# Kernel optimization log

Hardware: AMD Instinct MI355X
Metric: run time of the kernel (lower is better)

Reference implementation:

```python
import jax, jax.numpy as jnp
import numpy as np

N_VERTS = 20000
BATCH = 4
C_FEAT = 64
VOX = 64
N_FACES = 40000


def _lin(key, fan_in, fan_out):
    return jax.random.normal(key, (fan_in, fan_out), jnp.float32) / np.sqrt(fan_in)


def setup_inputs() -> dict:
    key = jax.random.key(0)
    ks = jax.random.split(key, 16)
    # faces -> unique directed edges, as in faces_to_edges (done host-side, static shape)
    rng = np.random.default_rng(0)
    faces = rng.integers(0, N_VERTS, (N_FACES, 3))
    e = np.concatenate([faces[:, :2], faces[:, 1:], faces[:, [0, 2]]], axis=0)
    e = np.unique(e, axis=0)
    edge_index = jnp.asarray(e.T, dtype=jnp.int32)  # [2, E]
    gdims = [(128, 256), (256, 512), (512, 1024), (1024, 512), (512, 256), (256, 128)]
    inp = {
        'features': jax.random.normal(ks[0], (BATCH, C_FEAT, VOX, VOX, VOX), jnp.float32),
        'vertices': jax.random.normal(ks[1], (N_VERTS, 3), jnp.float32),
        'edge_index': edge_index,
        'enc_W1': _lin(ks[2], 3 + C_FEAT, 256), 'enc_b1': jnp.zeros((256,), jnp.float32),
        'enc_W2': _lin(ks[3], 256, 128), 'enc_b2': jnp.zeros((128,), jnp.float32),
    }
    for i, (a, b) in enumerate(gdims):
        inp[f'gW{i+1}'] = _lin(ks[4 + i], a, b)
        inp[f'gb{i+1}'] = jnp.zeros((b,), jnp.float32)
    inp['hW1'] = _lin(ks[10], 128, 128); inp['hb1'] = jnp.zeros((128,), jnp.float32)
    inp['hW2'] = _lin(ks[11], 128, 64); inp['hb2'] = jnp.zeros((64,), jnp.float32)
    inp['hW3'] = _lin(ks[12], 64, 3); inp['hb3'] = jnp.zeros((3,), jnp.float32)
    return inp


def trilinear_sample(feat, grid):
    # feat [B,C,D,H,W]; grid [B,N,3] in [-1,1], channel order (x->W, y->H, z->D)
    # align_corners=True, padding_mode='border'
    _, C, D, H, W = feat.shape

    def per_sample(f, g):
        def un(c, s):
            return jnp.clip((c + 1.0) * 0.5 * (s - 1), 0.0, s - 1.0)
        x = un(g[:, 0], W); y = un(g[:, 1], H); z = un(g[:, 2], D)
        x0 = jnp.floor(x); y0 = jnp.floor(y); z0 = jnp.floor(z)
        wx = x - x0; wy = y - y0; wz = z - z0
        x0i = jnp.clip(x0.astype(jnp.int32), 0, W - 1); x1i = jnp.clip(x0i + 1, 0, W - 1)
        y0i = jnp.clip(y0.astype(jnp.int32), 0, H - 1); y1i = jnp.clip(y0i + 1, 0, H - 1)
        z0i = jnp.clip(z0.astype(jnp.int32), 0, D - 1); z1i = jnp.clip(z0i + 1, 0, D - 1)
        def g8(zi, yi, xi):
            return f[:, zi, yi, xi]  # [C,N]
        c00 = g8(z0i, y0i, x0i) * (1 - wx) + g8(z0i, y0i, x1i) * wx
        c01 = g8(z0i, y1i, x0i) * (1 - wx) + g8(z0i, y1i, x1i) * wx
        c10 = g8(z1i, y0i, x0i) * (1 - wx) + g8(z1i, y0i, x1i) * wx
        c11 = g8(z1i, y1i, x0i) * (1 - wx) + g8(z1i, y1i, x1i) * wx
        c0 = c00 * (1 - wy) + c01 * wy
        c1 = c10 * (1 - wy) + c11 * wy
        return (c0 * (1 - wz) + c1 * wz).T  # [N,C]

    return jax.vmap(per_sample)(feat, grid)


def _forward(features, vertices, edge_index,
             enc_W1, enc_b1, enc_W2, enc_b2,
             gWs, gbs, hW1, hb1, hW2, hb2, hW3, hb3):
    B = features.shape[0]
    N = vertices.shape[0]
    # sample_voxel_features: min/max over batch axis of identical copies -> constant grid
    vexp = jnp.broadcast_to(vertices[None], (B, N, 3))
    mn = vexp.min(axis=0, keepdims=True)
    mx = vexp.max(axis=0, keepdims=True)
    vn = 2.0 * (vexp - mn) / (mx - mn + 1e-6) - 1.0
    vn = vn / 1.5  # chamber == 0
    vfeat = trilinear_sample(features, vn)  # [B,N,C]
    x = jnp.concatenate([vexp, vfeat], axis=-1)
    x = jax.nn.relu(x @ enc_W1 + enc_b1)
    x = jax.nn.relu(x @ enc_W2 + enc_b2)  # [B,N,128]
    # PyG GCNConv: self-loops + symmetric normalization (bn layers unused in source forward)
    src = edge_index[0]
    dst = edge_index[1]
    deg = jnp.zeros((N,), x.dtype).at[dst].add(1.0) + 1.0  # includes self-loop
    dinv = 1.0 / jnp.sqrt(deg)
    nrm = dinv[src] * dinv[dst]  # [E]
    selfw = (dinv * dinv)[None, :, None]  # self-loop norm

    def gcn(h, W_, b_):
        h = h @ W_  # [B,N,Cout]
        agg = jnp.zeros_like(h).at[:, dst].add(h[:, src] * nrm[None, :, None])
        return jax.nn.relu(h * selfw + agg + b_)

    for W_, b_ in zip(gWs, gbs):
        x = gcn(x, W_, b_)
    d = jax.nn.relu(x @ hW1 + hb1)
    d = jax.nn.relu(d @ hW2 + hb2)
    d = jnp.tanh(d @ hW3 + hb3)
    d = jnp.nan_to_num(d, nan=0.0)
    return vertices[None] + jnp.clip(d, -2.5, 2.5)


def reference(features, vertices, edge_index,
              enc_W1, enc_b1, enc_W2, enc_b2,
              gW1, gb1, gW2, gb2, gW3, gb3, gW4, gb4, gW5, gb5, gW6, gb6,
              hW1, hb1, hW2, hb2, hW3, hb3):
    return _forward(features, vertices, edge_index,
                    enc_W1, enc_b1, enc_W2, enc_b2,
                    (gW1, gW2, gW3, gW4, gW5, gW6),
                    (gb1, gb2, gb3, gb4, gb5, gb6),
                    hW1, hb1, hW2, hb2, hW3, hb3)
```

## Files before the change

### kernel.cpp

```cpp
#include <hip/hip_runtime.h>
#include <math.h>

#define NV 20000
#define NV_PAD 20096
#define NB 4
#define M_TOTAL (NB * NV_PAD)
#define CF 64
#define VX 64

typedef short short8 __attribute__((ext_vector_type(8)));
typedef float floatx4 __attribute__((ext_vector_type(4)));

__device__ __forceinline__ float bf2f(unsigned int h) {
  return __uint_as_float(h << 16);
}
__device__ __forceinline__ unsigned short f2bf(float f) {
  unsigned int u = __float_as_uint(f);
  u += 0x7fffu + ((u >> 16) & 1u);
  return (unsigned short)(u >> 16);
}


__global__ void hist_dst_kernel(const int* __restrict__ dst, int E, int* __restrict__ cnt) {
  int i = blockIdx.x * blockDim.x + threadIdx.x;
  if (i < E) atomicAdd(&cnt[dst[i]], 1);
}

__global__ void scan_kernel(const int* __restrict__ cnt, int* __restrict__ rowp,
                            float* __restrict__ dinv, int n) {
  __shared__ int sdata[1024];
  __shared__ int run_s;
  if (threadIdx.x == 0) run_s = 0;
  __syncthreads();
  for (int base = 0; base < n; base += 1024) {
    int i = base + (int)threadIdx.x;
    int v = (i < n) ? cnt[i] : 0;
    sdata[threadIdx.x] = v;
    __syncthreads();
    int run = run_s;
    for (int ofs = 1; ofs < 1024; ofs <<= 1) {
      int t = (threadIdx.x >= (unsigned)ofs) ? sdata[threadIdx.x - ofs] : 0;
      __syncthreads();
      sdata[threadIdx.x] += t;
      __syncthreads();
    }
    if (i < n) {
      rowp[i] = run + sdata[threadIdx.x] - v;
      dinv[i] = 1.0f / sqrtf((float)(v + 1));
    }
    if (threadIdx.x == 1023) run_s = run + sdata[1023];
    __syncthreads();
  }
  if (threadIdx.x == 0) rowp[n] = run_s;
}

__global__ void fill_csr_kernel(const int* __restrict__ src, const int* __restrict__ dst, int E,
                                const int* __restrict__ rowp, int* __restrict__ cnt2,
                                const float* __restrict__ dinv,
                                int* __restrict__ esrc, float* __restrict__ dsrc) {
  int i = blockIdx.x * blockDim.x + threadIdx.x;
  if (i < E) {
    int d = dst[i];
    int s = src[i];
    int pos = rowp[d] + atomicAdd(&cnt2[d], 1);
    esrc[pos] = s;
    dsrc[pos] = dinv[s];
  }
}

__global__ void dinvrep_kernel(const float* __restrict__ dinv, float* __restrict__ drep) {
  int idx = blockIdx.x * blockDim.x + threadIdx.x;
  if (idx >= M_TOTAL) return;
  int n = idx % NV_PAD;
  drep[idx] = (n < NV) ? dinv[n] : 1.0f;
}

__global__ void vfeat_kernel(const float* __restrict__ feat, float* __restrict__ vfeat) {
  int t = blockIdx.x * blockDim.x + threadIdx.x;
  if (t >= NB * CF) return;
  float c = (2.0f * 0.0f / 1e-6f - 1.0f) / 1.5f;
  float pos = (c + 1.0f) * 0.5f * (float)(VX - 1);
  pos = fminf(fmaxf(pos, 0.0f), (float)(VX - 1));
  float f0 = floorf(pos);
  float w = pos - f0;
  int i0 = (int)f0;
  int i1 = i0 + 1; if (i1 > VX - 1) i1 = VX - 1;
  const float* base = feat + (size_t)t * VX * VX * VX;
  float wz[2] = {1.0f - w, w};
  int   iz[2] = {i0, i1};
  float acc = 0.0f;
  #pragma unroll
  for (int a = 0; a < 2; ++a)
    #pragma unroll
    for (int b = 0; b < 2; ++b)
      #pragma unroll
      for (int d = 0; d < 2; ++d)
        acc += wz[a] * wz[b] * wz[d] * base[(size_t)iz[a] * VX * VX + iz[b] * VX + iz[d]];
  vfeat[t] = acc;
}

__global__ void encconst_kernel(const float* __restrict__ vfeat, const float* __restrict__ W1,
                                const float* __restrict__ b1, float* __restrict__ encc) {
  int idx = blockIdx.x * blockDim.x + threadIdx.x;
  if (idx >= NB * 256) return;
  int b = idx >> 8, j = idx & 255;
  float acc = b1[j];
  #pragma unroll 8
  for (int c = 0; c < CF; ++c) acc += vfeat[b * CF + c] * W1[(3 + c) * 256 + j];
  encc[idx] = acc;
}

__global__ void enc1_kernel(const float* __restrict__ verts, const float* __restrict__ W1,
                            const float* __restrict__ encc, unsigned short* __restrict__ out) {
  int idx = blockIdx.x * blockDim.x + threadIdx.x;
  if (idx >= NV * 256) return;
  int n = idx >> 8, j = idx & 255;
  int b = blockIdx.y;
  float acc = encc[b * 256 + j]
            + verts[n * 3 + 0] * W1[0 * 256 + j]
            + verts[n * 3 + 1] * W1[1 * 256 + j]
            + verts[n * 3 + 2] * W1[2 * 256 + j];
  out[((size_t)(b * NV_PAD + n)) * 256 + j] = f2bf(fmaxf(acc, 0.0f));
}

struct WPrep {
  const float* src[9];
  unsigned short* dst[9];
};

__global__ void wprep_all_kernel(WPrep wp) {
  const int WKc[9] = {256, 128, 256, 512, 1024, 512, 256, 128, 128};
  const int WNc[9] = {128, 256, 512, 1024, 512, 256, 128, 128, 64};
  const int cum[10] = {0, 32768, 65536, 196608, 720896, 1245184, 1376256, 1409024, 1425408, 1433600};
  int idx = blockIdx.x * blockDim.x + threadIdx.x;
  if (idx >= 1433600) return;
  #pragma unroll
  for (int s = 0; s < 9; ++s) {
    if (idx >= cum[s] && idx < cum[s + 1]) {
      int local = idx - cum[s];
      int k = local / WNc[s];
      int n = local - k * WNc[s];
      wp.dst[s][(size_t)n * WKc[s] + k] = f2bf(wp.src[s][local]);
      return;
    }
  }
}

#define BM 128
#define BN 128
#define BK 32

__launch_bounds__(256, 4)
__global__ void gemm_bt_kernel(const unsigned short* __restrict__ A,
                               const unsigned short* __restrict__ Bt,
                               const float* __restrict__ bias,
                               const float* __restrict__ rowscale,
                               unsigned short* __restrict__ C,
                               int K, int Nreal, int flags) {
  __shared__ unsigned short As[BM * BK];
  __shared__ unsigned short Bs[BN * BK];
  int tid = threadIdx.x;
  int wave = tid >> 6, lane = tid & 63;

  unsigned int nwg = gridDim.x * gridDim.y;
  unsigned int orig = blockIdx.y * gridDim.x + blockIdx.x;
  unsigned int xcd = orig & 7u, pos = orig >> 3;
  unsigned int q = nwg >> 3, r = nwg & 7u;
  unsigned int wgid = (xcd < r ? xcd * (q + 1u) : r * (q + 1u) + (xcd - r) * q) + pos;
  unsigned int bx = wgid % gridDim.x;
  unsigned int by = wgid / gridDim.x;

  int mbase = by * BM;
  int nbase = bx * BN;
  int wm = (wave >> 1) * 64, wn = (wave & 1) * 64;

  floatx4 acc[4][4] = {};

  const int rowS = wave * 16 + (lane >> 2);
  const int sswz = ((lane >> 2) + (lane >> 4)) & 3;
  const int kseg = (((lane & 3) ^ sswz) << 3);
  const int fr = lane & 15, fq = lane >> 4;
  const int fswz = (fr + (fr >> 2)) & 3;
  const int fchunk = ((fq ^ fswz) << 3);

  for (int kb = 0; kb < K; kb += BK) {
    #pragma unroll
    for (int p = 0; p < 2; ++p) {
      const unsigned short* ga = A + (size_t)(mbase + rowS + p * 64) * K + kb + kseg;
      __builtin_amdgcn_global_load_lds(
          (const __attribute__((address_space(1))) void*)ga,
          (__attribute__((address_space(3))) void*)(As + wave * 512 + p * 2048), 16, 0, 0);
      const unsigned short* gb = Bt + (size_t)(nbase + rowS + p * 64) * K + kb + kseg;
      __builtin_amdgcn_global_load_lds(
          (const __attribute__((address_space(1))) void*)gb,
          (__attribute__((address_space(3))) void*)(Bs + wave * 512 + p * 2048), 16, 0, 0);
    }
    __syncthreads();
    short8 af[4], bf[4];
    #pragma unroll
    for (int i = 0; i < 4; ++i)
      af[i] = *(const short8*)(As + (wm + i * 16 + fr) * BK + fchunk);
    #pragma unroll
    for (int j = 0; j < 4; ++j)
      bf[j] = *(const short8*)(Bs + (wn + j * 16 + fr) * BK + fchunk);
    #pragma unroll
    for (int i = 0; i < 4; ++i)
      #pragma unroll
      for (int j = 0; j < 4; ++j)
        acc[i][j] = __builtin_amdgcn_mfma_f32_16x16x32_bf16(af[i], bf[j], acc[i][j], 0, 0, 0);
    __syncthreads();
  }

  #pragma unroll
  for (int j = 0; j < 4; ++j) {
    int n = nbase + wn + j * 16 + fr;
    if (n >= Nreal) continue;
    float bv = (flags & 1) ? bias[n] : 0.0f;
    #pragma unroll
    for (int i = 0; i < 4; ++i) {
      #pragma unroll
      for (int r = 0; r < 4; ++r) {
        int m = mbase + wm + i * 16 + fq * 4 + r;
        float v = acc[i][j][r];
        if (flags & 4) v *= rowscale[m];
        v += bv;
        if (flags & 2) v = fmaxf(v, 0.0f);
        C[(size_t)m * Nreal + n] = f2bf(v);
      }
    }
  }
}

__global__ void gcn_gather_kernel(const uint4* __restrict__ hs8,
                                  const float* __restrict__ bias,
                                  const float* __restrict__ dinv,
                                  const int* __restrict__ rowp, const int* __restrict__ esrc,
                                  uint4* __restrict__ out, int lc8) {
  int idx = blockIdx.x * blockDim.x + threadIdx.x;
  int C8 = 1 << lc8;
  if (idx >= NV * C8) return;
  int n = idx >> lc8;
  int j = idx & (C8 - 1);
  size_t rowbase = (size_t)blockIdx.y * NV_PAD;
  uint4 u = hs8[((rowbase + n) << lc8) + j];
  float a0 = bf2f(u.x & 0xffff), a1 = bf2f(u.x >> 16);
  float a2 = bf2f(u.y & 0xffff), a3 = bf2f(u.y >> 16);
  float a4 = bf2f(u.z & 0xffff), a5 = bf2f(u.z >> 16);
  float a6 = bf2f(u.w & 0xffff), a7 = bf2f(u.w >> 16);
  int s = rowp[n], e = rowp[n + 1];
  int t = s;
  int src = (t < e) ? esrc[t] : 0;
  while (t < e) {
    uint4 v = hs8[((rowbase + src) << lc8) + j];
    ++t;
    int src_n = (t < e) ? esrc[t] : 0;
    a0 += bf2f(v.x & 0xffff); a1 += bf2f(v.x >> 16);
    a2 += bf2f(v.y & 0xffff); a3 += bf2f(v.y >> 16);
    a4 += bf2f(v.z & 0xffff); a5 += bf2f(v.z >> 16);
    a6 += bf2f(v.w & 0xffff); a7 += bf2f(v.w >> 16);
    src = src_n;
  }
  float dn = dinv[n];
  int j8 = j << 3;
  a0 = fmaxf(a0 * dn + bias[j8 + 0], 0.0f);
  a1 = fmaxf(a1 * dn + bias[j8 + 1], 0.0f);
  a2 = fmaxf(a2 * dn + bias[j8 + 2], 0.0f);
  a3 = fmaxf(a3 * dn + bias[j8 + 3], 0.0f);
  a4 = fmaxf(a4 * dn + bias[j8 + 4], 0.0f);
  a5 = fmaxf(a5 * dn + bias[j8 + 5], 0.0f);
  a6 = fmaxf(a6 * dn + bias[j8 + 6], 0.0f);
  a7 = fmaxf(a7 * dn + bias[j8 + 7], 0.0f);
  uint4 o;
  o.x = (unsigned int)f2bf(a0) | ((unsigned int)f2bf(a1) << 16);
  o.y = (unsigned int)f2bf(a2) | ((unsigned int)f2bf(a3) << 16);
  o.z = (unsigned int)f2bf(a4) | ((unsigned int)f2bf(a5) << 16);
  o.w = (unsigned int)f2bf(a6) | ((unsigned int)f2bf(a7) << 16);
  out[((rowbase + n) << lc8) + j] = o;
}

__global__ void gcn_pre_gather_kernel(const uint4* __restrict__ x8,
                                      const float* __restrict__ dinv,
                                      const int* __restrict__ rowp, const int* __restrict__ esrc,
                                      const float* __restrict__ dsrc,
                                      uint4* __restrict__ out, int lc8) {
  int idx = blockIdx.x * blockDim.x + threadIdx.x;
  int C8 = 1 << lc8;
  if (idx >= NV * C8) return;
  int n = idx >> lc8;
  int j = idx & (C8 - 1);
  size_t rowbase = (size_t)blockIdx.y * NV_PAD;
  float dn = dinv[n];
  uint4 u = x8[((rowbase + n) << lc8) + j];
  float a0 = dn * bf2f(u.x & 0xffff), a1 = dn * bf2f(u.x >> 16);
  float a2 = dn * bf2f(u.y & 0xffff), a3 = dn * bf2f(u.y >> 16);
  float a4 = dn * bf2f(u.z & 0xffff), a5 = dn * bf2f(u.z >> 16);
  float a6 = dn * bf2f(u.w & 0xffff), a7 = dn * bf2f(u.w >> 16);
  int s = rowp[n], e = rowp[n + 1];
  int t = s;
  int src = (t < e) ? esrc[t] : 0;
  float w = (t < e) ? dsrc[t] : 0.0f;
  while (t < e) {
    uint4 v = x8[((rowbase + src) << lc8) + j];
    float wv = w;
    ++t;
    src = (t < e) ? esrc[t] : 0;
    w = (t < e) ? dsrc[t] : 0.0f;
    a0 += wv * bf2f(v.x & 0xffff); a1 += wv * bf2f(v.x >> 16);
    a2 += wv * bf2f(v.y & 0xffff); a3 += wv * bf2f(v.y >> 16);
    a4 += wv * bf2f(v.z & 0xffff); a5 += wv * bf2f(v.z >> 16);
    a6 += wv * bf2f(v.w & 0xffff); a7 += wv * bf2f(v.w >> 16);
  }
  a0 *= dn; a1 *= dn; a2 *= dn; a3 *= dn;
  a4 *= dn; a5 *= dn; a6 *= dn; a7 *= dn;
  uint4 o;
  o.x = (unsigned int)f2bf(a0) | ((unsigned int)f2bf(a1) << 16);
  o.y = (unsigned int)f2bf(a2) | ((unsigned int)f2bf(a3) << 16);
  o.z = (unsigned int)f2bf(a4) | ((unsigned int)f2bf(a5) << 16);
  o.w = (unsigned int)f2bf(a6) | ((unsigned int)f2bf(a7) << 16);
  out[((rowbase + n) << lc8) + j] = o;
}

__global__ void head3_kernel(const unsigned short* __restrict__ d, const float* __restrict__ hW3,
                             const float* __restrict__ hb3, const float* __restrict__ verts,
                             float* __restrict__ out) {
  int idx = blockIdx.x * blockDim.x + threadIdx.x;
  if (idx >= NV * 3) return;
  int n = idx / 3;
  int k = idx - n * 3;
  int b = blockIdx.y;
  const unsigned short* drow = d + ((size_t)(b * NV_PAD + n)) * 64;
  float acc = hb3[k];
  #pragma unroll 8
  for (int c = 0; c < 64; ++c) acc += bf2f(drow[c]) * hW3[c * 3 + k];
  float t = tanhf(acc);
  t = fminf(fmaxf(t, -2.5f), 2.5f);
  out[(size_t)b * NV * 3 + idx] = verts[idx] + t;
}


static inline void launch_gemm(const unsigned short* A, const unsigned short* Bt,
                               const float* bias, const float* rowscale, unsigned short* C,
                               int N, int K, int flags, hipStream_t stream) {
  int Npad = (N + BN - 1) / BN * BN;
  dim3 grid(Npad / BN, M_TOTAL / BM);
  gemm_bt_kernel<<<grid, 256, 0, stream>>>(A, Bt, bias, rowscale, C, K, N, flags);
}

extern "C" void kernel_launch(void* const* d_in, const int* in_sizes, int n_in,
                              void* d_out, int out_size, void* d_ws, size_t ws_size,
                              hipStream_t stream) {
  const float* features = (const float*)d_in[0];
  const float* vertices = (const float*)d_in[1];
  const int* edge_index = (const int*)d_in[2];
  const int E = in_sizes[2] / 2;
  const int* esrc_in = edge_index;
  const int* edst_in = edge_index + E;
  const float* enc_W1 = (const float*)d_in[3];
  const float* enc_b1 = (const float*)d_in[4];
  const float* enc_W2 = (const float*)d_in[5];
  const float* enc_b2 = (const float*)d_in[6];
  const float* gW[6]; const float* gb[6];
  for (int i = 0; i < 6; ++i) { gW[i] = (const float*)d_in[7 + 2 * i]; gb[i] = (const float*)d_in[8 + 2 * i]; }
  const float* hW1 = (const float*)d_in[19]; const float* hb1 = (const float*)d_in[20];
  const float* hW2 = (const float*)d_in[21]; const float* hb2 = (const float*)d_in[22];
  const float* hW3 = (const float*)d_in[23]; const float* hb3 = (const float*)d_in[24];

  char* ws = (char*)d_ws;
  size_t off = 0;
  auto alloc = [&](size_t bytes) -> void* {
    void* p = (void*)(ws + off);
    off += (bytes + 255) & ~(size_t)255;
    return p;
  };
  unsigned short* bufA = (unsigned short*)alloc((size_t)M_TOTAL * 1024 * 2);
  unsigned short* bufB = (unsigned short*)alloc((size_t)M_TOTAL * 1024 * 2);
  float* dinv  = (float*)alloc(NV * sizeof(float));
  float* drep  = (float*)alloc(M_TOTAL * sizeof(float));
  float* vfeat = (float*)alloc(NB * CF * sizeof(float));
  float* encc  = (float*)alloc(NB * 256 * sizeof(float));
  int* cnt  = (int*)alloc(NV * sizeof(int));
  int* rowp = (int*)alloc((NV + 1) * sizeof(int));
  int* cnt2 = (int*)alloc(NV * sizeof(int));
  int* esrc = (int*)alloc((size_t)E * sizeof(int));
  float* dsrc = (float*)alloc((size_t)E * sizeof(float));
  const size_t wtsz[9] = {128 * 256, 256 * 128, 512 * 256, 1024 * 512, 512 * 1024,
                          256 * 512, 128 * 256, 128 * 128, 128 * 128};
  unsigned short* wt[9];
  {
    size_t tot = 0;
    for (int i = 0; i < 9; ++i) tot += wtsz[i];
    unsigned short* base = (unsigned short*)alloc(tot * 2);
    size_t o = 0;
    for (int i = 0; i < 9; ++i) { wt[i] = base + o; o += wtsz[i]; }
  }

  hipMemsetAsync(cnt,  0, NV * sizeof(int), stream);
  hipMemsetAsync(cnt2, 0, NV * sizeof(int), stream);
  hist_dst_kernel<<<(E + 255) / 256, 256, 0, stream>>>(edst_in, E, cnt);
  scan_kernel<<<1, 1024, 0, stream>>>(cnt, rowp, dinv, NV);
  fill_csr_kernel<<<(E + 255) / 256, 256, 0, stream>>>(esrc_in, edst_in, E, rowp, cnt2,
                                                       dinv, esrc, dsrc);
  dinvrep_kernel<<<(M_TOTAL + 255) / 256, 256, 0, stream>>>(dinv, drep);
  vfeat_kernel<<<1, 256, 0, stream>>>(features, vfeat);
  encconst_kernel<<<NB, 256, 0, stream>>>(vfeat, enc_W1, enc_b1, encc);

  WPrep wp;
  const float* wsrc[9] = {enc_W2, gW[0], gW[1], gW[2], gW[3], gW[4], gW[5], hW1, hW2};
  for (int i = 0; i < 9; ++i) { wp.src[i] = wsrc[i]; wp.dst[i] = wt[i]; }
  wprep_all_kernel<<<(1433600 + 255) / 256, 256, 0, stream>>>(wp);

  const int gout[6] = {256, 512, 1024, 512, 256, 128};
  const int gin[6]  = {128, 256, 512, 1024, 512, 256};
  const int inlc8[6] = {4, 5, 6, 7, 6, 5};
  const int outlc8[6] = {5, 6, 7, 6, 5, 4};
  const int inside[6] = {1, 1, 1, 0, 0, 0};

  dim3 e1grid((NV * 256 + 255) / 256, NB);
  enc1_kernel<<<e1grid, 256, 0, stream>>>(vertices, enc_W1, encc, bufA);
  launch_gemm(bufA, wt[0], enc_b2, nullptr, bufB, 128, 256, 1 | 2, stream);

  unsigned short* x = bufB;
  unsigned short* h = bufA;
  for (int i = 0; i < 6; ++i) {
    if (inside[i]) {
      int total8 = NV * (gin[i] / 8);
      dim3 pgrid((total8 + 255) / 256, NB);
      gcn_pre_gather_kernel<<<pgrid, 256, 0, stream>>>(
          (const uint4*)x, dinv, rowp, esrc, dsrc, (uint4*)h, inlc8[i]);
      launch_gemm(h, wt[1 + i], gb[i], nullptr, x, gout[i], gin[i], 1 | 2, stream);
    } else {
      launch_gemm(x, wt[1 + i], nullptr, drep, h, gout[i], gin[i], 4, stream);
      int total8 = NV * (gout[i] / 8);
      dim3 ggrid((total8 + 255) / 256, NB);
      gcn_gather_kernel<<<ggrid, 256, 0, stream>>>(
          (const uint4*)h, gb[i], dinv, rowp, esrc, (uint4*)x, outlc8[i]);
    }
  }
  launch_gemm(x, wt[7], hb1, nullptr, h, 128, 128, 1 | 2, stream);
  launch_gemm(h, wt[8], hb2, nullptr, x, 64, 128, 1 | 2, stream);
  dim3 hgrid((NV * 3 + 255) / 256, NB);
  head3_kernel<<<hgrid, 256, 0, stream>>>(x, hW3, hb3, vertices, (float*)d_out);
}
```

Measured before the change: 1.177 ms.

## Double-buffer GEMM LDS tiles and batch-fuse GCN gather kernels

The GEMM kernel now double-buffers its A/B LDS tiles, issuing the global-to-LDS loads for the next K step before computing on the current one. This hides load latency and leaves one barrier per iteration instead of two, at the cost of doubled LDS use, which may lower occupancy. Both GCN gather kernels now have each thread handle all four batch items, so CSR row pointers, edge indices and weights are read once per vertex instead of once per batch. The batch grid dimension is removed in exchange for more registers per thread and fewer threads in flight.

```diff
diff --git a/kernel.cpp b/kernel.cpp
--- a/kernel.cpp
+++ b/kernel.cpp
@@ -157,8 +157,8 @@
                                const float* __restrict__ rowscale,
                                unsigned short* __restrict__ C,
                                int K, int Nreal, int flags) {
-  __shared__ unsigned short As[BM * BK];
-  __shared__ unsigned short Bs[BN * BK];
+  __shared__ unsigned short As[2 * BM * BK];
+  __shared__ unsigned short Bs[2 * BM * BK];
   int tid = threadIdx.x;
   int wave = tid >> 6, lane = tid & 63;
 
@@ -183,32 +183,45 @@
   const int fswz = (fr + (fr >> 2)) & 3;
   const int fchunk = ((fq ^ fswz) << 3);
 
-  for (int kb = 0; kb < K; kb += BK) {
+  const unsigned short* ga0 = A + (size_t)(mbase + rowS) * K + kseg;
+  const unsigned short* gb0 = Bt + (size_t)(nbase + rowS) * K + kseg;
+
+  auto stage = [&](int kb, int half) {
     #pragma unroll
     for (int p = 0; p < 2; ++p) {
-      const unsigned short* ga = A + (size_t)(mbase + rowS + p * 64) * K + kb + kseg;
       __builtin_amdgcn_global_load_lds(
-          (const __attribute__((address_space(1))) void*)ga,
-          (__attribute__((address_space(3))) void*)(As + wave * 512 + p * 2048), 16, 0, 0);
-      const unsigned short* gb = Bt + (size_t)(nbase + rowS + p * 64) * K + kb + kseg;
+          (const __attribute__((address_space(1))) void*)(ga0 + (size_t)(p * 64) * K + kb),
+          (__attribute__((address_space(3))) void*)(As + half * 4096 + wave * 512 + p * 2048),
+          16, 0, 0);
       __builtin_amdgcn_global_load_lds(
-          (const __attribute__((address_space(1))) void*)gb,
-          (__attribute__((address_space(3))) void*)(Bs + wave * 512 + p * 2048), 16, 0, 0);
+          (const __attribute__((address_space(1))) void*)(gb0 + (size_t)(p * 64) * K + kb),
+          (__attribute__((address_space(3))) void*)(Bs + half * 4096 + wave * 512 + p * 2048),
+          16, 0, 0);
     }
-    __syncthreads();
+  };
+
+  const int nt = K / BK;
+  stage(0, 0);
+  __syncthreads();
+  int cur = 0;
+  for (int t = 0; t < nt; ++t) {
+    if (t + 1 < nt) stage((t + 1) * BK, cur ^ 1);
+    const unsigned short* as = As + cur * 4096;
+    const unsigned short* bs = Bs + cur * 4096;
     short8 af[4], bf[4];
     #pragma unroll
     for (int i = 0; i < 4; ++i)
-      af[i] = *(const short8*)(As + (wm + i * 16 + fr) * BK + fchunk);
+      af[i] = *(const short8*)(as + (wm + i * 16 + fr) * BK + fchunk);
     #pragma unroll
     for (int j = 0; j < 4; ++j)
-      bf[j] = *(const short8*)(Bs + (wn + j * 16 + fr) * BK + fchunk);
+      bf[j] = *(const short8*)(bs + (wn + j * 16 + fr) * BK + fchunk);
     #pragma unroll
     for (int i = 0; i < 4; ++i)
       #pragma unroll
       for (int j = 0; j < 4; ++j)
         acc[i][j] = __builtin_amdgcn_mfma_f32_16x16x32_bf16(af[i], bf[j], acc[i][j], 0, 0, 0);
     __syncthreads();
+    cur ^= 1;
   }
 
   #pragma unroll
@@ -241,41 +254,66 @@
   if (idx >= NV * C8) return;
   int n = idx >> lc8;
   int j = idx & (C8 - 1);
-  size_t rowbase = (size_t)blockIdx.y * NV_PAD;
-  uint4 u = hs8[((rowbase + n) << lc8) + j];
-  float a0 = bf2f(u.x & 0xffff), a1 = bf2f(u.x >> 16);
-  float a2 = bf2f(u.y & 0xffff), a3 = bf2f(u.y >> 16);
-  float a4 = bf2f(u.z & 0xffff), a5 = bf2f(u.z >> 16);
-  float a6 = bf2f(u.w & 0xffff), a7 = bf2f(u.w >> 16);
+  const size_t bstride = (size_t)NV_PAD << lc8;
+  float a[NB][8];
+  #pragma unroll
+  for (int b = 0; b < NB; ++b) {
+    uint4 u = hs8[b * bstride + ((size_t)n << lc8) + j];
+    a[b][0] = bf2f(u.x & 0xffff); a[b][1] = bf2f(u.x >> 16);
+    a[b][2] = bf2f(u.y & 0xffff); a[b][3] = bf2f(u.y >> 16);
+    a[b][4] = bf2f(u.z & 0xffff); a[b][5] = bf2f(u.z >> 16);
+    a[b][6] = bf2f(u.w & 0xffff); a[b][7] = bf2f(u.w >> 16);
+  }
   int s = rowp[n], e = rowp[n + 1];
   int t = s;
   int src = (t < e) ? esrc[t] : 0;
   while (t < e) {
-    uint4 v = hs8[((rowbase + src) << lc8) + j];
+    size_t rb = ((size_t)src << lc8) + j;
+    uint4 v0 = hs8[rb];
+    uint4 v1 = hs8[rb + bstride];
+    uint4 v2 = hs8[rb + 2 * bstride];
+    uint4 v3 = hs8[rb + 3 * bstride];
     ++t;
-    int src_n = (t < e) ? esrc[t] : 0;
-    a0 += bf2f(v.x & 0xffff); a1 += bf2f(v.x >> 16);
-    a2 += bf2f(v.y & 0xffff); a3 += bf2f(v.y >> 16);
-    a4 += bf2f(v.z & 0xffff); a5 += bf2f(v.z >> 16);
-    a6 += bf2f(v.w & 0xffff); a7 += bf2f(v.w >> 16);
-    src = src_n;
+    src = (t < e) ? esrc[t] : 0;
+    a[0][0] += bf2f(v0.x & 0xffff); a[0][1] += bf2f(v0.x >> 16);
+    a[0][2] += bf2f(v0.y & 0xffff); a[0][3] += bf2f(v0.y >> 16);
+    a[0][4] += bf2f(v0.z & 0xffff); a[0][5] += bf2f(v0.z >> 16);
+    a[0][6] += bf2f(v0.w & 0xffff); a[0][7] += bf2f(v0.w >> 16);
+    a[1][0] += bf2f(v1.x & 0xffff); a[1][1] += bf2f(v1.x >> 16);
+    a[1][2] += bf2f(v1.y & 0xffff); a[1][3] += bf2f(v1.y >> 16);
+    a[1][4] += bf2f(v1.z & 0xffff); a[1][5] += bf2f(v1.z >> 16);
+    a[1][6] += bf2f(v1.w & 0xffff); a[1][7] += bf2f(v1.w >> 16);
+    a[2][0] += bf2f(v2.x & 0xffff); a[2][1] += bf2f(v2.x >> 16);
+    a[2][2] += bf2f(v2.y & 0xffff); a[2][3] += bf2f(v2.y >> 16);
+    a[2][4] += bf2f(v2.z & 0xffff); a[2][5] += bf2f(v2.z >> 16);
+    a[2][6] += bf2f(v2.w & 0xffff); a[2][7] += bf2f(v2.w >> 16);
+    a[3][0] += bf2f(v3.x & 0xffff); a[3][1] += bf2f(v3.x >> 16);
+    a[3][2] += bf2f(v3.y & 0xffff); a[3][3] += bf2f(v3.y >> 16);
+    a[3][4] += bf2f(v3.z & 0xffff); a[3][5] += bf2f(v3.z >> 16);
+    a[3][6] += bf2f(v3.w & 0xffff); a[3][7] += bf2f(v3.w >> 16);
   }
   float dn = dinv[n];
   int j8 = j << 3;
-  a0 = fmaxf(a0 * dn + bias[j8 + 0], 0.0f);
-  a1 = fmaxf(a1 * dn + bias[j8 + 1], 0.0f);
-  a2 = fmaxf(a2 * dn + bias[j8 + 2], 0.0f);
-  a3 = fmaxf(a3 * dn + bias[j8 + 3], 0.0f);
-  a4 = fmaxf(a4 * dn + bias[j8 + 4], 0.0f);
-  a5 = fmaxf(a5 * dn + bias[j8 + 5], 0.0f);
-  a6 = fmaxf(a6 * dn + bias[j8 + 6], 0.0f);
-  a7 = fmaxf(a7 * dn + bias[j8 + 7], 0.0f);
-  uint4 o;
-  o.x = (unsigned int)f2bf(a0) | ((unsigned int)f2bf(a1) << 16);
-  o.y = (unsigned int)f2bf(a2) | ((unsigned int)f2bf(a3) << 16);
-  o.z = (unsigned int)f2bf(a4) | ((unsigned int)f2bf(a5) << 16);
-  o.w = (unsigned int)f2bf(a6) | ((unsigned int)f2bf(a7) << 16);
-  out[((rowbase + n) << lc8) + j] = o;
+  float bb[8];
+  #pragma unroll
+  for (int c = 0; c < 8; ++c) bb[c] = bias[j8 + c];
+  #pragma unroll
+  for (int b = 0; b < NB; ++b) {
+    uint4 o;
+    float r0 = fmaxf(a[b][0] * dn + bb[0], 0.0f);
+    float r1 = fmaxf(a[b][1] * dn + bb[1], 0.0f);
+    float r2 = fmaxf(a[b][2] * dn + bb[2], 0.0f);
+    float r3 = fmaxf(a[b][3] * dn + bb[3], 0.0f);
+    float r4 = fmaxf(a[b][4] * dn + bb[4], 0.0f);
+    float r5 = fmaxf(a[b][5] * dn + bb[5], 0.0f);
+    float r6 = fmaxf(a[b][6] * dn + bb[6], 0.0f);
+    float r7 = fmaxf(a[b][7] * dn + bb[7], 0.0f);
+    o.x = (unsigned int)f2bf(r0) | ((unsigned int)f2bf(r1) << 16);
+    o.y = (unsigned int)f2bf(r2) | ((unsigned int)f2bf(r3) << 16);
+    o.z = (unsigned int)f2bf(r4) | ((unsigned int)f2bf(r5) << 16);
+    o.w = (unsigned int)f2bf(r6) | ((unsigned int)f2bf(r7) << 16);
+    out[b * bstride + ((size_t)n << lc8) + j] = o;
+  }
 }
 
 __global__ void gcn_pre_gather_kernel(const uint4* __restrict__ x8,
@@ -288,36 +326,57 @@
   if (idx >= NV * C8) return;
   int n = idx >> lc8;
   int j = idx & (C8 - 1);
-  size_t rowbase = (size_t)blockIdx.y * NV_PAD;
+  const size_t bstride = (size_t)NV_PAD << lc8;
   float dn = dinv[n];
-  uint4 u = x8[((rowbase + n) << lc8) + j];
-  float a0 = dn * bf2f(u.x & 0xffff), a1 = dn * bf2f(u.x >> 16);
-  float a2 = dn * bf2f(u.y & 0xffff), a3 = dn * bf2f(u.y >> 16);
-  float a4 = dn * bf2f(u.z & 0xffff), a5 = dn * bf2f(u.z >> 16);
-  float a6 = dn * bf2f(u.w & 0xffff), a7 = dn * bf2f(u.w >> 16);
+  float a[NB][8];
+  #pragma unroll
+  for (int b = 0; b < NB; ++b) {
+    uint4 u = x8[b * bstride + ((size_t)n << lc8) + j];
+    a[b][0] = dn * bf2f(u.x & 0xffff); a[b][1] = dn * bf2f(u.x >> 16);
+    a[b][2] = dn * bf2f(u.y & 0xffff); a[b][3] = dn * bf2f(u.y >> 16);
+    a[b][4] = dn * bf2f(u.z & 0xffff); a[b][5] = dn * bf2f(u.z >> 16);
+    a[b][6] = dn * bf2f(u.w & 0xffff); a[b][7] = dn * bf2f(u.w >> 16);
+  }
   int s = rowp[n], e = rowp[n + 1];
   int t = s;
   int src = (t < e) ? esrc[t] : 0;
   float w = (t < e) ? dsrc[t] : 0.0f;
   while (t < e) {
-    uint4 v = x8[((rowbase + src) << lc8) + j];
+    size_t rb = ((size_t)src << lc8) + j;
+    uint4 v0 = x8[rb];
+    uint4 v1 = x8[rb + bstride];
+    uint4 v2 = x8[rb + 2 * bstride];
+    uint4 v3 = x8[rb + 3 * bstride];
     float wv = w;
     ++t;
     src = (t < e) ? esrc[t] : 0;
     w = (t < e) ? dsrc[t] : 0.0f;
-    a0 += wv * bf2f(v.x & 0xffff); a1 += wv * bf2f(v.x >> 16);
-    a2 += wv * bf2f(v.y & 0xffff); a3 += wv * bf2f(v.y >> 16);
-    a4 += wv * bf2f(v.z & 0xffff); a5 += wv * bf2f(v.z >> 16);
-    a6 += wv * bf2f(v.w & 0xffff); a7 += wv * bf2f(v.w >> 16);
-  }
-  a0 *= dn; a1 *= dn; a2 *= dn; a3 *= dn;
-  a4 *= dn; a5 *= dn; a6 *= dn; a7 *= dn;
-  uint4 o;
-  o.x = (unsigned int)f2bf(a0) | ((unsigned int)f2bf(a1) << 16);
-  o.y = (unsigned int)f2bf(a2) | ((unsigned int)f2bf(a3) << 16);
-  o.z = (unsigned int)f2bf(a4) | ((unsigned int)f2bf(a5) << 16);
-  o.w = (unsigned int)f2bf(a6) | ((unsigned int)f2bf(a7) << 16);
-  out[((rowbase + n) << lc8) + j] = o;
+    a[0][0] += wv * bf2f(v0.x & 0xffff); a[0][1] += wv * bf2f(v0.x >> 16);
+    a[0][2] += wv * bf2f(v0.y & 0xffff); a[0][3] += wv * bf2f(v0.y >> 16);
+    a[0][4] += wv * bf2f(v0.z & 0xffff); a[0][5] += wv * bf2f(v0.z >> 16);
+    a[0][6] += wv * bf2f(v0.w & 0xffff); a[0][7] += wv * bf2f(v0.w >> 16);
+    a[1][0] += wv * bf2f(v1.x & 0xffff); a[1][1] += wv * bf2f(v1.x >> 16);
+    a[1][2] += wv * bf2f(v1.y & 0xffff); a[1][3] += wv * bf2f(v1.y >> 16);
+    a[1][4] += wv * bf2f(v1.z & 0xffff); a[1][5] += wv * bf2f(v1.z >> 16);
+    a[1][6] += wv * bf2f(v1.w & 0xffff); a[1][7] += wv * bf2f(v1.w >> 16);
+    a[2][0] += wv * bf2f(v2.x & 0xffff); a[2][1] += wv * bf2f(v2.x >> 16);
+    a[2][2] += wv * bf2f(v2.y & 0xffff); a[2][3] += wv * bf2f(v2.y >> 16);
+    a[2][4] += wv * bf2f(v2.z & 0xffff); a[2][5] += wv * bf2f(v2.z >> 16);
+    a[2][6] += wv * bf2f(v2.w & 0xffff); a[2][7] += wv * bf2f(v2.w >> 16);
+    a[3][0] += wv * bf2f(v3.x & 0xffff); a[3][1] += wv * bf2f(v3.x >> 16);
+    a[3][2] += wv * bf2f(v3.y & 0xffff); a[3][3] += wv * bf2f(v3.y >> 16);
+    a[3][4] += wv * bf2f(v3.z & 0xffff); a[3][5] += wv * bf2f(v3.z >> 16);
+    a[3][6] += wv * bf2f(v3.w & 0xffff); a[3][7] += wv * bf2f(v3.w >> 16);
+  }
+  #pragma unroll
+  for (int b = 0; b < NB; ++b) {
+    uint4 o;
+    o.x = (unsigned int)f2bf(a[b][0] * dn) | ((unsigned int)f2bf(a[b][1] * dn) << 16);
+    o.y = (unsigned int)f2bf(a[b][2] * dn) | ((unsigned int)f2bf(a[b][3] * dn) << 16);
+    o.z = (unsigned int)f2bf(a[b][4] * dn) | ((unsigned int)f2bf(a[b][5] * dn) << 16);
+    o.w = (unsigned int)f2bf(a[b][6] * dn) | ((unsigned int)f2bf(a[b][7] * dn) << 16);
+    out[b * bstride + ((size_t)n << lc8) + j] = o;
+  }
 }
 
 __global__ void head3_kernel(const unsigned short* __restrict__ d, const float* __restrict__ hW3,
@@ -424,15 +483,13 @@
   for (int i = 0; i < 6; ++i) {
     if (inside[i]) {
       int total8 = NV * (gin[i] / 8);
-      dim3 pgrid((total8 + 255) / 256, NB);
-      gcn_pre_gather_kernel<<<pgrid, 256, 0, stream>>>(
+      gcn_pre_gather_kernel<<<(total8 + 255) / 256, 256, 0, stream>>>(
           (const uint4*)x, dinv, rowp, esrc, dsrc, (uint4*)h, inlc8[i]);
       launch_gemm(h, wt[1 + i], gb[i], nullptr, x, gout[i], gin[i], 1 | 2, stream);
     } else {
       launch_gemm(x, wt[1 + i], nullptr, drep, h, gout[i], gin[i], 4, stream);
       int total8 = NV * (gout[i] / 8);
-      dim3 ggrid((total8 + 255) / 256, NB);
-      gcn_gather_kernel<<<ggrid, 256, 0, stream>>>(
+      gcn_gather_kernel<<<(total8 + 255) / 256, 256, 0, stream>>>(
           (const uint4*)h, gb[i], dinv, rowp, esrc, (uint4*)x, outlc8[i]);
     }
   }
```

Result: no change. 1.199 ms (+1.9%).
